# Performance work log

Hardware: AMD Instinct MI355X
Metric: run time of the kernel (lower is better)

Reference implementation:

```python
import jax, jax.numpy as jnp
import numpy as np

N, C, H, E = 10000, 128, 256, 320000
CUTOFF = 5.0
EPS = 1e-5


def _ln(x, g, b):
    mu = jnp.mean(x, axis=-1, keepdims=True)
    var = jnp.var(x, axis=-1, keepdims=True)
    return (x - mu) * jax.lax.rsqrt(var + EPS) * g + b


def setup_inputs() -> dict:
    key = jax.random.key(0)
    ks = jax.random.split(key, 24)

    def w(k, shape, fan_in):
        return (jax.random.normal(k, shape, dtype=jnp.float32) / np.sqrt(fan_in)).astype(jnp.float32)

    inp = {}
    inp["x"] = jax.random.normal(ks[0], (N, 3), dtype=jnp.float32)
    inp["h"] = jax.random.normal(ks[1], (N, C), dtype=jnp.float32)
    inp["edge_index"] = jax.random.randint(ks[2], (2, E), 0, N, dtype=jnp.int32)
    # edge_mlp: Linear(2C+1 -> H), SiLU, Linear(H -> H), SiLU
    inp["We1"] = w(ks[3], (2 * C + 1, H), 2 * C + 1); inp["be1"] = jnp.zeros((H,), jnp.float32)
    inp["We2"] = w(ks[4], (H, H), H);                inp["be2"] = jnp.zeros((H,), jnp.float32)
    # node_mlp: Linear(C+H -> H), SiLU, Linear(H -> C)
    inp["Wn1"] = w(ks[5], (C + H, H), C + H);        inp["bn1"] = jnp.zeros((H,), jnp.float32)
    inp["Wn2"] = w(ks[6], (H, C), H);                inp["bn2"] = jnp.zeros((C,), jnp.float32)
    # residual mlp: Linear(C -> H), SiLU, Dropout(eval), Linear(H -> C)
    inp["Wm1"] = w(ks[7], (C, H), C);                inp["bm1"] = jnp.zeros((H,), jnp.float32)
    inp["Wm2"] = w(ks[8], (H, C), H);                inp["bm2"] = jnp.zeros((C,), jnp.float32)
    # layernorms
    inp["g1"] = jnp.ones((C,), jnp.float32); inp["beta1"] = jnp.zeros((C,), jnp.float32)
    inp["g2"] = jnp.ones((C,), jnp.float32); inp["beta2"] = jnp.zeros((C,), jnp.float32)
    return inp


def reference(x, h, edge_index, We1, be1, We2, be2, Wn1, bn1, Wn2, bn2,
              Wm1, bm1, Wm2, bm2, g1, beta1, g2, beta2):
    row, col = edge_index[0], edge_index[1]

    h_res = h
    hn = _ln(h, g1, beta1)                              # [N, C]

    # ---- EGNN layer ----
    rel = x[row] - x[col]                               # [E, 3]
    dist = jnp.linalg.norm(rel, axis=-1, keepdims=True) # [E, 1]
    edge_in = jnp.concatenate([hn[row], hn[col], dist], axis=-1)  # [E, 2C+1]
    m = jax.nn.silu(edge_in @ We1 + be1)
    m = jax.nn.silu(m @ We2 + be2)                      # [E, H]

    d = dist[:, 0]
    Ccut = 0.5 * (jnp.cos(d * jnp.pi / CUTOFF) + 1.0)
    Ccut = Ccut * (d <= CUTOFF) * (d >= 0.0)
    m = m * Ccut[:, None]

    # mean-aggregate messages at target nodes (edge_index[1])
    sums = jax.ops.segment_sum(m, col, num_segments=N)          # [N, H]
    cnt = jax.ops.segment_sum(jnp.ones((m.shape[0],), m.dtype), col, num_segments=N)
    m_aggr = sums / jnp.maximum(cnt, 1.0)[:, None]

    hd = jax.nn.silu(jnp.concatenate([hn, m_aggr], axis=-1) @ Wn1 + bn1) @ Wn2 + bn2
    h_egnn = hn + hd

    h1 = h_res + h_egnn

    # ---- norm2 + MLP residual (dropout = identity in eval) ----
    h2 = _ln(h1, g2, beta2)
    h2 = jax.nn.silu(h2 @ Wm1 + bm1) @ Wm2 + bm2
    return h1 + h2
```

## Files before the change

kernel.cpp:

```cpp
#include <hip/hip_runtime.h>

#define NN 10000
#define CC 128
#define HH 256
#define EE 320000
#define ETILE 128

typedef __bf16 bf16_t;
typedef __bf16 bf16x8 __attribute__((ext_vector_type(8)));
typedef __bf16 bf16x4 __attribute__((ext_vector_type(4)));
typedef __bf16 bf16x2 __attribute__((ext_vector_type(2)));
typedef float f32x4 __attribute__((ext_vector_type(4)));

__device__ __forceinline__ float silu_f(float v) {
#if __has_builtin(__builtin_amdgcn_rcpf)
  return v * __builtin_amdgcn_rcpf(1.0f + __expf(-v));
#else
  return v / (1.0f + __expf(-v));
#endif
}


template<int RE, int KD, int SA, int NT>
__device__ __forceinline__ void gemm_lg(const bf16_t* sAa, const bf16_t* __restrict__ BT,
                                        int nwavebase, int lr, int quad, f32x4 acc[RE][NT]) {
  for (int kk = 0; kk < KD; kk += 32) {
    bf16x8 a[RE]; bf16x8 b[NT];
#pragma unroll
    for (int re = 0; re < RE; re++)
      a[re] = *(const bf16x8*)(sAa + (re * 16 + lr) * SA + kk + quad * 8);
#pragma unroll
    for (int ce = 0; ce < NT; ce++)
      b[ce] = *(const bf16x8*)(BT + (size_t)(nwavebase + ce * 16 + lr) * KD + kk + quad * 8);
#pragma unroll
    for (int re = 0; re < RE; re++)
#pragma unroll
      for (int ce = 0; ce < NT; ce++)
        acc[re][ce] = __builtin_amdgcn_mfma_f32_16x16x32_bf16(a[re], b[ce], acc[re][ce], 0, 0, 0);
  }
}

template<int KD, int SB, int NE>
__device__ __forceinline__ void gemm_gl(const bf16_t* __restrict__ AT, int mwavebase,
                                        const bf16_t* sB, int lr, int quad, f32x4 acc[4][NE]) {
  for (int kk = 0; kk < KD; kk += 32) {
    bf16x8 a[4]; bf16x8 b[NE];
#pragma unroll
    for (int re = 0; re < 4; re++)
      a[re] = *(const bf16x8*)(AT + (size_t)(mwavebase + re * 16 + lr) * KD + kk + quad * 8);
#pragma unroll
    for (int ce = 0; ce < NE; ce++)
      b[ce] = *(const bf16x8*)(sB + (ce * 16 + lr) * SB + kk + quad * 8);
#pragma unroll
    for (int re = 0; re < 4; re++)
#pragma unroll
      for (int ce = 0; ce < NE; ce++)
        acc[re][ce] = __builtin_amdgcn_mfma_f32_16x16x32_bf16(a[re], b[ce], acc[re][ce], 0, 0, 0);
  }
}

__global__ __launch_bounds__(256) void prep_weights(
    const float* __restrict__ We1, const float* __restrict__ We2,
    const float* __restrict__ Wn1, const float* __restrict__ Wn2,
    const float* __restrict__ Wm1, const float* __restrict__ Wm2,
    bf16_t* __restrict__ We1T, bf16_t* __restrict__ We2T,
    bf16_t* __restrict__ Wn1T, bf16_t* __restrict__ Wn2T,
    bf16_t* __restrict__ Wm1T, bf16_t* __restrict__ Wm2T) {
  int i = blockIdx.x * 256 + threadIdx.x;
  const float* src; bf16_t* dst; int K, Nc, idx;
  if      (i < 65536)  { src = We1; dst = We1T; K = 256; Nc = 256; idx = i; }
  else if (i < 131072) { src = We2; dst = We2T; K = 256; Nc = 256; idx = i - 65536; }
  else if (i < 229376) { src = Wn1; dst = Wn1T; K = 384; Nc = 256; idx = i - 131072; }
  else if (i < 262144) { src = Wn2; dst = Wn2T; K = 256; Nc = 128; idx = i - 229376; }
  else if (i < 294912) { src = Wm1; dst = Wm1T; K = 128; Nc = 256; idx = i - 262144; }
  else                 { src = Wm2; dst = Wm2T; K = 256; Nc = 128; idx = i - 294912; }
  int n = idx / K, k = idx - n * K;
  dst[idx] = (bf16_t)src[(size_t)k * Nc + n];
}

__global__ __launch_bounds__(256) void ln1_kernel(const float* __restrict__ src,
                                                  const float* __restrict__ g,
                                                  const float* __restrict__ b,
                                                  bf16_t* __restrict__ out16) {
  int node = blockIdx.x * 4 + (threadIdx.x >> 6);
  int lane = threadIdx.x & 63;
  size_t base = (size_t)node * CC;
  float v1 = src[base + lane], v2 = src[base + lane + 64];
  float s = v1 + v2, sq = v1 * v1 + v2 * v2;
#pragma unroll
  for (int o = 32; o > 0; o >>= 1) { s += __shfl_xor(s, o); sq += __shfl_xor(sq, o); }
  float mu = s * (1.0f / CC);
  float var = sq * (1.0f / CC) - mu * mu;
  float rs = rsqrtf(var + 1e-5f);
  out16[base + lane] = (bf16_t)((v1 - mu) * rs * g[lane] + b[lane]);
  out16[base + lane + 64] = (bf16_t)((v2 - mu) * rs * g[lane + 64] + b[lane + 64]);
}

__global__ __launch_bounds__(256) void count_kernel(const int* __restrict__ ei, int* __restrict__ cnt) {
  int e = blockIdx.x * 256 + threadIdx.x;
  atomicAdd(&cnt[ei[EE + e]], 1);
}

__global__ __launch_bounds__(1024) void scan_kernel(const int* __restrict__ cnt, int* __restrict__ cursor) {
  __shared__ int wsum[16];
  int tid = threadIdx.x, wave = tid >> 6, lane = tid & 63;
  int base = 0;
  for (int start = 0; start < NN; start += 1024) {
    int i = start + tid;
    int v = (i < NN) ? cnt[i] : 0;
    int s = v;
#pragma unroll
    for (int off = 1; off < 64; off <<= 1) { int t = __shfl_up(s, off); if (lane >= off) s += t; }
    if (lane == 63) wsum[wave] = s;
    __syncthreads();
    if (tid < 16) {
      int ws = wsum[tid];
#pragma unroll
      for (int off = 1; off < 16; off <<= 1) { int t = __shfl_up(ws, off); if (tid >= off) ws += t; }
      wsum[tid] = ws;
    }
    __syncthreads();
    int wp = (wave > 0) ? wsum[wave - 1] : 0;
    if (i < NN) cursor[i] = base + wp + s - v;
    base += wsum[15];
    __syncthreads();
  }
}

__global__ __launch_bounds__(256) void scatter_kernel(const int* __restrict__ ei,
                                                      const float* __restrict__ x,
                                                      int* __restrict__ cursor,
                                                      uint4* __restrict__ edat) {
  int e = blockIdx.x * 256 + threadIdx.x;
  int r = ei[e], c = ei[EE + e];
  float dx = x[3 * r] - x[3 * c];
  float dy = x[3 * r + 1] - x[3 * c + 1];
  float dz = x[3 * r + 2] - x[3 * c + 2];
  float d = sqrtf(dx * dx + dy * dy + dz * dz);
  float cc = (d <= 5.0f) ? 0.5f * (cosf(d * 0.6283185307179586f) + 1.0f) : 0.0f;
  int pos = atomicAdd(&cursor[c], 1);
  uint4 v = {(unsigned)r, (unsigned)c, __float_as_uint(d), __float_as_uint(cc)};
  edat[pos] = v;
}

__global__ __launch_bounds__(256, 2) void edge_mlp_kernel(
    const uint4* __restrict__ edat, const bf16_t* __restrict__ hn16,
    const bf16_t* __restrict__ We1T, const float* __restrict__ We1last,
    const float* __restrict__ be1,
    const bf16_t* __restrict__ We2T, const float* __restrict__ be2,
    float* __restrict__ sums) {
  __shared__ __align__(16) bf16_t sBuf[ETILE * 264];
  __shared__ int sRow[ETILE], sCol[ETILE];
  __shared__ float sD[ETILE], sCc[ETILE];
  __shared__ int sSegStart[ETILE + 1];
  __shared__ int sNseg;
  __shared__ unsigned long long sMask[2];
  int tid = threadIdx.x;
  int lane = tid & 63, wave = tid >> 6;
  int lr = lane & 15, quad = lane >> 4;
  int e0 = blockIdx.x * ETILE;

  if (tid < ETILE) {
    uint4 v = edat[e0 + tid];
    sRow[tid] = (int)v.x; sCol[tid] = (int)v.y;
    sD[tid] = __uint_as_float(v.z); sCc[tid] = __uint_as_float(v.w);
  }
  __syncthreads();

  if (tid < ETILE) {
    int fl = (tid > 0) && (sCol[tid] != sCol[tid - 1]);
    unsigned long long m = __ballot(fl);
    if ((tid & 63) == 0) sMask[wave] = m;
  }

#pragma unroll
  for (int i = 0; i < 16; i++) {
    int o = tid + i * 256;
    int e = o >> 5, q = o & 31;
    int srcrow = (q < 16) ? sRow[e] : sCol[e];
    uint4 v = *(const uint4*)(hn16 + (size_t)srcrow * CC + (q & 15) * 8);
    *(uint4*)(sBuf + e * 264 + (q & 15) * 8 + ((q < 16) ? 0 : 128)) = v;
  }
  __syncthreads();

  f32x4 zf = {0.f, 0.f, 0.f, 0.f};
  {
    f32x4 acc[4][8];
#pragma unroll
    for (int i = 0; i < 4; i++)
#pragma unroll
      for (int j = 0; j < 8; j++) acc[i][j] = zf;
    gemm_gl<256, 264, 8>(We1T, wave * 64, sBuf, lr, quad, acc);
    __syncthreads();

#pragma unroll
    for (int re = 0; re < 4; re++) {
      int nb = wave * 64 + re * 16 + quad * 4;
      f32x4 b1 = *(const f32x4*)(be1 + nb);
      f32x4 wl = *(const f32x4*)(We1last + nb);
#pragma unroll
      for (int ce = 0; ce < 8; ce++) {
        int e = ce * 16 + lr;
        float d = sD[e];
        bf16x4 o;
#pragma unroll
        for (int r = 0; r < 4; r++)
          o[r] = (bf16_t)silu_f(acc[re][ce][r] + b1[r] + d * wl[r]);
        *(bf16x4*)(sBuf + e * 264 + nb) = o;
      }
    }
  }
  __syncthreads();

  {
    f32x4 acc[8][4];
#pragma unroll
    for (int i = 0; i < 8; i++)
#pragma unroll
      for (int j = 0; j < 4; j++) acc[i][j] = zf;
    gemm_lg<8, 256, 264, 4>(sBuf, We2T, wave * 64, lr, quad, acc);
    __syncthreads();

#pragma unroll
    for (int re = 0; re < 8; re++) {
      int eb = re * 16 + quad * 4;
      f32x4 cc = *(const f32x4*)(sCc + eb);
#pragma unroll
      for (int ce = 0; ce < 4; ce++) {
        int n = wave * 64 + ce * 16 + lr;
        float b2 = be2[n];
        float v0 = silu_f(acc[re][ce][0] + b2) * cc[0];
        float v1 = silu_f(acc[re][ce][1] + b2) * cc[1];
        float v2 = silu_f(acc[re][ce][2] + b2) * cc[2];
        float v3 = silu_f(acc[re][ce][3] + b2) * cc[3];
        bf16x2 p0 = {(bf16_t)v0, (bf16_t)v1};
        bf16x2 p1 = {(bf16_t)v2, (bf16_t)v3};
        *(bf16x2*)(sBuf + n * 130 + eb) = p0;
        *(bf16x2*)(sBuf + n * 130 + eb + 2) = p1;
      }
    }
  }

  if (tid < ETILE) {
    unsigned long long m0 = sMask[0], m1 = sMask[1];
    int fl = (tid > 0) && (sCol[tid] != sCol[tid - 1]);
    if (fl) {
      int l = tid & 63;
      unsigned long long below = ((tid < 64) ? m0 : m1) & ((1ull << l) - 1ull);
      int idx = __popcll(below) + ((tid >= 64) ? __popcll(m0) : 0) + 1;
      sSegStart[idx] = tid;
    }
    if (tid == 0) {
      int ns = 1 + __popcll(m0) + __popcll(m1);
      sNseg = ns;
      sSegStart[0] = 0;
      sSegStart[ns] = ETILE;
    }
  }
  __syncthreads();

  {
    int nseg = sNseg;
    const bf16_t* rowp = sBuf + tid * 130;
    for (int s = 0; s < nseg; s++) {
      int lo = sSegStart[s], hi = sSegStart[s + 1];
      int colv = sCol[lo];
      float a = 0.0f;
      int e = lo;
      if (e & 1) { a += (float)rowp[e]; e++; }
      for (; e + 1 < hi; e += 2) {
        unsigned w = *(const unsigned*)(rowp + e);
        a += __uint_as_float(w << 16) + __uint_as_float(w & 0xffff0000u);
      }
      if (e < hi) a += (float)rowp[e];
      atomicAdd(&sums[(size_t)colv * HH + tid], a);
    }
  }
}

__global__ __launch_bounds__(256) void node_fused_kernel(
    const float* __restrict__ h, const bf16_t* __restrict__ hn16,
    const float* __restrict__ sums, const int* __restrict__ cnt,
    const bf16_t* __restrict__ Wn1T, const float* __restrict__ bn1,
    const bf16_t* __restrict__ Wn2T, const float* __restrict__ bn2,
    const float* __restrict__ g2, const float* __restrict__ bt2,
    const bf16_t* __restrict__ Wm1T, const float* __restrict__ bm1,
    const bf16_t* __restrict__ Wm2T, const float* __restrict__ bm2,
    float* __restrict__ out) {
  __shared__ __align__(16) bf16_t sA1[16 * 392];
  __shared__ __align__(16) bf16_t sM[16 * 264];
  __shared__ __align__(16) float sH1[16 * 132];
  __shared__ __align__(16) bf16_t sLn[16 * 136];
  __shared__ float sRc[16];
  int tid = threadIdx.x;
  int lane = tid & 63, wave = tid >> 6;
  int lr = lane & 15, quad = lane >> 4;
  int n0 = blockIdx.x * 16;

  if (tid < 16) sRc[tid] = 1.0f / fmaxf((float)cnt[n0 + tid], 1.0f);
  __syncthreads();

#pragma unroll
  for (int i = 0; i < 3; i++) {
    int o = tid + i * 256;
    int e = o / 48, q = o - e * 48;
    int node = n0 + e;
    if (q < 16) {
      *(uint4*)(sA1 + e * 392 + q * 8) = *(const uint4*)(hn16 + (size_t)node * CC + q * 8);
    } else {
      float rc = sRc[e];
      const float* sp = sums + (size_t)node * HH + (q - 16) * 8;
      bf16x8 bv;
#pragma unroll
      for (int k2 = 0; k2 < 8; k2++) bv[k2] = (bf16_t)(sp[k2] * rc);
      *(bf16x8*)(sA1 + e * 392 + (q - 16) * 8 + 128) = bv;
    }
  }
  __syncthreads();

  f32x4 zf = {0.f, 0.f, 0.f, 0.f};
  {
    f32x4 acc[1][4];
#pragma unroll
    for (int j = 0; j < 4; j++) acc[0][j] = zf;
    gemm_lg<1, 384, 392, 4>(sA1, Wn1T, wave * 64, lr, quad, acc);
#pragma unroll
    for (int ce = 0; ce < 4; ce++) {
      int n = wave * 64 + ce * 16 + lr;
      float b1 = bn1[n];
#pragma unroll
      for (int r = 0; r < 4; r++)
        sM[(quad * 4 + r) * 264 + n] = (bf16_t)silu_f(acc[0][ce][r] + b1);
    }
  }
  __syncthreads();

  {
    f32x4 acc[1][2];
    acc[0][0] = zf; acc[0][1] = zf;
    gemm_lg<1, 256, 264, 2>(sM, Wn2T, wave * 32, lr, quad, acc);
#pragma unroll
    for (int ce = 0; ce < 2; ce++) {
      int n = wave * 32 + ce * 16 + lr;
      float b2 = bn2[n];
#pragma unroll
      for (int r = 0; r < 4; r++) {
        int node = quad * 4 + r;
        size_t idx = (size_t)(n0 + node) * CC + n;
        float hn_v = (float)sA1[node * 392 + n];
        sH1[node * 132 + n] = h[idx] + hn_v + acc[0][ce][r] + b2;
      }
    }
  }
  __syncthreads();

  {
    int node = tid >> 4, c0 = (tid & 15) * 8;
    f32x4 u0 = *(const f32x4*)(sH1 + node * 132 + c0);
    f32x4 u1 = *(const f32x4*)(sH1 + node * 132 + c0 + 4);
    float s = 0.f, sq = 0.f;
#pragma unroll
    for (int j = 0; j < 4; j++) { s += u0[j] + u1[j]; sq += u0[j] * u0[j] + u1[j] * u1[j]; }
#pragma unroll
    for (int o = 8; o > 0; o >>= 1) { s += __shfl_xor(s, o); sq += __shfl_xor(sq, o); }
    float mu = s * (1.0f / CC);
    float var = sq * (1.0f / CC) - mu * mu;
    float rs = rsqrtf(var + 1e-5f);
    f32x4 gg0 = *(const f32x4*)(g2 + c0), gg1 = *(const f32x4*)(g2 + c0 + 4);
    f32x4 bb0 = *(const f32x4*)(bt2 + c0), bb1 = *(const f32x4*)(bt2 + c0 + 4);
    bf16x8 ov;
#pragma unroll
    for (int j = 0; j < 4; j++) {
      ov[j] = (bf16_t)((u0[j] - mu) * rs * gg0[j] + bb0[j]);
      ov[j + 4] = (bf16_t)((u1[j] - mu) * rs * gg1[j] + bb1[j]);
    }
    *(bf16x8*)(sLn + node * 136 + c0) = ov;
  }
  __syncthreads();

  {
    f32x4 acc[1][4];
#pragma unroll
    for (int j = 0; j < 4; j++) acc[0][j] = zf;
    gemm_lg<1, 128, 136, 4>(sLn, Wm1T, wave * 64, lr, quad, acc);
#pragma unroll
    for (int ce = 0; ce < 4; ce++) {
      int n = wave * 64 + ce * 16 + lr;
      float b1 = bm1[n];
#pragma unroll
      for (int r = 0; r < 4; r++)
        sM[(quad * 4 + r) * 264 + n] = (bf16_t)silu_f(acc[0][ce][r] + b1);
    }
  }
  __syncthreads();

  {
    f32x4 acc[1][2];
    acc[0][0] = zf; acc[0][1] = zf;
    gemm_lg<1, 256, 264, 2>(sM, Wm2T, wave * 32, lr, quad, acc);
#pragma unroll
    for (int ce = 0; ce < 2; ce++) {
      int n = wave * 32 + ce * 16 + lr;
      float b2 = bm2[n];
#pragma unroll
      for (int r = 0; r < 4; r++) {
        int node = quad * 4 + r;
        size_t idx = (size_t)(n0 + node) * CC + n;
        out[idx] = sH1[node * 132 + n] + acc[0][ce][r] + b2;
      }
    }
  }
}

extern "C" void kernel_launch(void* const* d_in, const int* in_sizes, int n_in,
                              void* d_out, int out_size, void* d_ws, size_t ws_size,
                              hipStream_t stream) {
  const float* x    = (const float*)d_in[0];
  const float* h    = (const float*)d_in[1];
  const int*   ei   = (const int*)d_in[2];
  const float* We1  = (const float*)d_in[3];
  const float* be1  = (const float*)d_in[4];
  const float* We2  = (const float*)d_in[5];
  const float* be2  = (const float*)d_in[6];
  const float* Wn1  = (const float*)d_in[7];
  const float* bn1  = (const float*)d_in[8];
  const float* Wn2  = (const float*)d_in[9];
  const float* bn2  = (const float*)d_in[10];
  const float* Wm1  = (const float*)d_in[11];
  const float* bm1  = (const float*)d_in[12];
  const float* Wm2  = (const float*)d_in[13];
  const float* bm2  = (const float*)d_in[14];
  const float* g1   = (const float*)d_in[15];
  const float* bt1  = (const float*)d_in[16];
  const float* g2   = (const float*)d_in[17];
  const float* bt2  = (const float*)d_in[18];
  float* out = (float*)d_out;

  char* wp = (char*)d_ws;
  size_t off = 0;
  auto alloc = [&](size_t bytes) -> void* {
    void* p = wp + off;
    off = (off + bytes + 255) & ~(size_t)255;
    return p;
  };

  bf16_t* hn16   = (bf16_t*)alloc((size_t)NN * CC * 2);
  float*  sums   = (float*)alloc((size_t)NN * HH * 4);
  int*    cnt    = (int*)alloc((size_t)NN * 4);
  int*    cursor = (int*)alloc((size_t)NN * 4);
  uint4*  edat   = (uint4*)alloc((size_t)EE * 16);
  bf16_t* We1T   = (bf16_t*)alloc(256 * 256 * 2);
  bf16_t* We2T   = (bf16_t*)alloc(256 * 256 * 2);
  bf16_t* Wn1T   = (bf16_t*)alloc(256 * 384 * 2);
  bf16_t* Wn2T   = (bf16_t*)alloc(128 * 256 * 2);
  bf16_t* Wm1T   = (bf16_t*)alloc(256 * 128 * 2);
  bf16_t* Wm2T   = (bf16_t*)alloc(128 * 256 * 2);

  hipMemsetAsync(sums, 0, (size_t)NN * HH * 4, stream);
  hipMemsetAsync(cnt, 0, (size_t)NN * 4, stream);

  prep_weights<<<1280, 256, 0, stream>>>(We1, We2, Wn1, Wn2, Wm1, Wm2,
                                         We1T, We2T, Wn1T, Wn2T, Wm1T, Wm2T);

  ln1_kernel<<<NN / 4, 256, 0, stream>>>(h, g1, bt1, hn16);

  count_kernel<<<EE / 256, 256, 0, stream>>>(ei, cnt);
  scan_kernel<<<1, 1024, 0, stream>>>(cnt, cursor);
  scatter_kernel<<<EE / 256, 256, 0, stream>>>(ei, x, cursor, edat);

  edge_mlp_kernel<<<EE / ETILE, 256, 0, stream>>>(edat, hn16,
                                                  We1T, We1 + 256 * 256, be1,
                                                  We2T, be2, sums);

  node_fused_kernel<<<NN / 16, 256, 0, stream>>>(h, hn16, sums, cnt,
                                                 Wn1T, bn1, Wn2T, bn2,
                                                 g2, bt2, Wm1T, bm1, Wm2T, bm2, out);
}
```

Baseline: 347.3 us.

## Factor first edge-MLP layer into per-node projections and reduce segments in registers

The first edge layer is linear over the concatenation [hn[row], hn[col], dist], so it is split into two per-node projections. A new node_pre_kernel fuses LayerNorm with computing P = hn·We1[:C] + be1 and Q = hn·We1[C:2C], and the edge kernel only gathers P[row] + Q[col] + d·w_last before SiLU. This replaces an E×256×256 GEMM with an N-sized one. It also removes the shared-memory transpose for segment sums by reducing each segment in MFMA accumulator registers with shuffles, and retiles edges to 96 per block, zero-padding the sorted edge buffer. The cost is an extra bf16 PQ buffer read with random gathers, plus some rounding from storing P and Q in bf16 before the add.

```diff
diff --git a/kernel.cpp b/kernel.cpp
--- a/kernel.cpp
+++ b/kernel.cpp
@@ -4,12 +4,12 @@
 #define CC 128
 #define HH 256
 #define EE 320000
-#define ETILE 128
+#define ETILE 96
+#define EBLOCKS 3334
 
 typedef __bf16 bf16_t;
 typedef __bf16 bf16x8 __attribute__((ext_vector_type(8)));
 typedef __bf16 bf16x4 __attribute__((ext_vector_type(4)));
-typedef __bf16 bf16x2 __attribute__((ext_vector_type(2)));
 typedef float f32x4 __attribute__((ext_vector_type(4)));
 
 __device__ __forceinline__ float silu_f(float v) {
@@ -20,7 +20,6 @@
 #endif
 }
 
-
 template<int RE, int KD, int SA, int NT>
 __device__ __forceinline__ void gemm_lg(const bf16_t* sAa, const bf16_t* __restrict__ BT,
                                         int nwavebase, int lr, int quad, f32x4 acc[RE][NT]) {
@@ -36,25 +35,6 @@
     for (int re = 0; re < RE; re++)
 #pragma unroll
       for (int ce = 0; ce < NT; ce++)
-        acc[re][ce] = __builtin_amdgcn_mfma_f32_16x16x32_bf16(a[re], b[ce], acc[re][ce], 0, 0, 0);
-  }
-}
-
-template<int KD, int SB, int NE>
-__device__ __forceinline__ void gemm_gl(const bf16_t* __restrict__ AT, int mwavebase,
-                                        const bf16_t* sB, int lr, int quad, f32x4 acc[4][NE]) {
-  for (int kk = 0; kk < KD; kk += 32) {
-    bf16x8 a[4]; bf16x8 b[NE];
-#pragma unroll
-    for (int re = 0; re < 4; re++)
-      a[re] = *(const bf16x8*)(AT + (size_t)(mwavebase + re * 16 + lr) * KD + kk + quad * 8);
-#pragma unroll
-    for (int ce = 0; ce < NE; ce++)
-      b[ce] = *(const bf16x8*)(sB + (ce * 16 + lr) * SB + kk + quad * 8);
-#pragma unroll
-    for (int re = 0; re < 4; re++)
-#pragma unroll
-      for (int ce = 0; ce < NE; ce++)
         acc[re][ce] = __builtin_amdgcn_mfma_f32_16x16x32_bf16(a[re], b[ce], acc[re][ce], 0, 0, 0);
   }
 }
@@ -78,22 +58,101 @@
   dst[idx] = (bf16_t)src[(size_t)k * Nc + n];
 }
 
-__global__ __launch_bounds__(256) void ln1_kernel(const float* __restrict__ src,
-                                                  const float* __restrict__ g,
-                                                  const float* __restrict__ b,
-                                                  bf16_t* __restrict__ out16) {
-  int node = blockIdx.x * 4 + (threadIdx.x >> 6);
-  int lane = threadIdx.x & 63;
-  size_t base = (size_t)node * CC;
-  float v1 = src[base + lane], v2 = src[base + lane + 64];
-  float s = v1 + v2, sq = v1 * v1 + v2 * v2;
-#pragma unroll
-  for (int o = 32; o > 0; o >>= 1) { s += __shfl_xor(s, o); sq += __shfl_xor(sq, o); }
-  float mu = s * (1.0f / CC);
-  float var = sq * (1.0f / CC) - mu * mu;
-  float rs = rsqrtf(var + 1e-5f);
-  out16[base + lane] = (bf16_t)((v1 - mu) * rs * g[lane] + b[lane]);
-  out16[base + lane + 64] = (bf16_t)((v2 - mu) * rs * g[lane + 64] + b[lane + 64]);
+__global__ __launch_bounds__(256, 3) void node_pre_kernel(
+    const float* __restrict__ h, const float* __restrict__ g1,
+    const float* __restrict__ bt1,
+    const bf16_t* __restrict__ We1T, const float* __restrict__ be1,
+    bf16_t* __restrict__ hn16, bf16_t* __restrict__ PQ) {
+  __shared__ __align__(16) float sHf[64 * 132];
+  __shared__ __align__(16) bf16_t sHn[64 * 136];
+  int tid = threadIdx.x;
+  int lane = tid & 63, wave = tid >> 6;
+  int lr = lane & 15, quad = lane >> 4;
+  int n0 = blockIdx.x * 64;
+
+#pragma unroll
+  for (int i = 0; i < 8; i++) {
+    int o = tid + i * 256;
+    int node = o >> 5, q = o & 31;
+    f32x4 v = {0.f, 0.f, 0.f, 0.f};
+    if (n0 + node < NN) v = *(const f32x4*)(h + (size_t)(n0 + node) * CC + q * 4);
+    *(f32x4*)(sHf + node * 132 + q * 4) = v;
+  }
+  __syncthreads();
+
+  {
+    int node = tid >> 2, c0 = (tid & 3) * 32;
+    f32x4 u[8];
+    float s = 0.f, sq = 0.f;
+#pragma unroll
+    for (int j = 0; j < 8; j++) {
+      u[j] = *(const f32x4*)(sHf + node * 132 + c0 + j * 4);
+#pragma unroll
+      for (int r = 0; r < 4; r++) { s += u[j][r]; sq += u[j][r] * u[j][r]; }
+    }
+    s += __shfl_xor(s, 1); sq += __shfl_xor(sq, 1);
+    s += __shfl_xor(s, 2); sq += __shfl_xor(sq, 2);
+    float mu = s * (1.0f / CC);
+    float var = sq * (1.0f / CC) - mu * mu;
+    float rs = rsqrtf(var + 1e-5f);
+    bool live = (n0 + node) < NN;
+#pragma unroll
+    for (int j2 = 0; j2 < 4; j2++) {
+      f32x4 gg0 = *(const f32x4*)(g1 + c0 + j2 * 8);
+      f32x4 gg1 = *(const f32x4*)(g1 + c0 + j2 * 8 + 4);
+      f32x4 bb0 = *(const f32x4*)(bt1 + c0 + j2 * 8);
+      f32x4 bb1 = *(const f32x4*)(bt1 + c0 + j2 * 8 + 4);
+      bf16x8 ov;
+#pragma unroll
+      for (int r = 0; r < 4; r++) {
+        ov[r] = (bf16_t)((u[j2 * 2][r] - mu) * rs * gg0[r] + bb0[r]);
+        ov[r + 4] = (bf16_t)((u[j2 * 2 + 1][r] - mu) * rs * gg1[r] + bb1[r]);
+      }
+      *(bf16x8*)(sHn + node * 136 + c0 + j2 * 8) = ov;
+      if (live) *(bf16x8*)(hn16 + (size_t)(n0 + node) * CC + c0 + j2 * 8) = ov;
+    }
+  }
+  __syncthreads();
+
+  f32x4 zf = {0.f, 0.f, 0.f, 0.f};
+#pragma unroll
+  for (int p = 0; p < 2; p++) {
+    f32x4 acc[4][4];
+#pragma unroll
+    for (int i = 0; i < 4; i++)
+#pragma unroll
+      for (int j = 0; j < 4; j++) acc[i][j] = zf;
+    for (int kk = 0; kk < 128; kk += 32) {
+      bf16x8 a[4]; bf16x8 b[4];
+#pragma unroll
+      for (int re = 0; re < 4; re++)
+        a[re] = *(const bf16x8*)(We1T + (size_t)(wave * 64 + re * 16 + lr) * 256 + p * 128 + kk + quad * 8);
+#pragma unroll
+      for (int ce = 0; ce < 4; ce++)
+        b[ce] = *(const bf16x8*)(sHn + (ce * 16 + lr) * 136 + kk + quad * 8);
+#pragma unroll
+      for (int re = 0; re < 4; re++)
+#pragma unroll
+        for (int ce = 0; ce < 4; ce++)
+          acc[re][ce] = __builtin_amdgcn_mfma_f32_16x16x32_bf16(a[re], b[ce], acc[re][ce], 0, 0, 0);
+    }
+#pragma unroll
+    for (int re = 0; re < 4; re++) {
+      int cbase = wave * 64 + re * 16 + quad * 4;
+      f32x4 bb = zf;
+      if (p == 0) bb = *(const f32x4*)(be1 + cbase);
+#pragma unroll
+      for (int ce = 0; ce < 4; ce++) {
+        int node = ce * 16 + lr;
+        if (n0 + node < NN) {
+          bf16x4 o;
+#pragma unroll
+          for (int r = 0; r < 4; r++) o[r] = (bf16_t)(acc[re][ce][r] + bb[r]);
+          *(bf16x4*)(PQ + (size_t)(n0 + node) * 512 + p * 256 + cbase) = o;
+        }
+      }
+    }
+  }
 }
 
 __global__ __launch_bounds__(256) void count_kernel(const int* __restrict__ ei, int* __restrict__ cnt) {
@@ -143,17 +202,14 @@
   edat[pos] = v;
 }
 
-__global__ __launch_bounds__(256, 2) void edge_mlp_kernel(
-    const uint4* __restrict__ edat, const bf16_t* __restrict__ hn16,
-    const bf16_t* __restrict__ We1T, const float* __restrict__ We1last,
-    const float* __restrict__ be1,
+__global__ __launch_bounds__(256, 3) void edge_mlp_kernel(
+    const uint4* __restrict__ edat, const bf16_t* __restrict__ PQ,
+    const float* __restrict__ We1last,
     const bf16_t* __restrict__ We2T, const float* __restrict__ be2,
     float* __restrict__ sums) {
-  __shared__ __align__(16) bf16_t sBuf[ETILE * 264];
+  __shared__ __align__(16) bf16_t sM1[ETILE * 264];
   __shared__ int sRow[ETILE], sCol[ETILE];
   __shared__ float sD[ETILE], sCc[ETILE];
-  __shared__ int sSegStart[ETILE + 1];
-  __shared__ int sNseg;
   __shared__ unsigned long long sMask[2];
   int tid = threadIdx.x;
   int lane = tid & 63, wave = tid >> 6;
@@ -174,106 +230,86 @@
   }
 
 #pragma unroll
-  for (int i = 0; i < 16; i++) {
+  for (int i = 0; i < ETILE * 32 / 256; i++) {
     int o = tid + i * 256;
     int e = o >> 5, q = o & 31;
-    int srcrow = (q < 16) ? sRow[e] : sCol[e];
-    uint4 v = *(const uint4*)(hn16 + (size_t)srcrow * CC + (q & 15) * 8);
-    *(uint4*)(sBuf + e * 264 + (q & 15) * 8 + ((q < 16) ? 0 : 128)) = v;
+    int k0 = q * 8;
+    int row = sRow[e], col = sCol[e];
+    float d = sD[e];
+    bf16x8 pv = *(const bf16x8*)(PQ + (size_t)row * 512 + k0);
+    bf16x8 qv = *(const bf16x8*)(PQ + (size_t)col * 512 + 256 + k0);
+    f32x4 wl0 = *(const f32x4*)(We1last + k0);
+    f32x4 wl1 = *(const f32x4*)(We1last + k0 + 4);
+    bf16x8 m;
+#pragma unroll
+    for (int j = 0; j < 4; j++) {
+      m[j] = (bf16_t)silu_f((float)pv[j] + (float)qv[j] + d * wl0[j]);
+      m[j + 4] = (bf16_t)silu_f((float)pv[j + 4] + (float)qv[j + 4] + d * wl1[j]);
+    }
+    *(bf16x8*)(sM1 + e * 264 + k0) = m;
   }
   __syncthreads();
 
   f32x4 zf = {0.f, 0.f, 0.f, 0.f};
-  {
-    f32x4 acc[4][8];
-#pragma unroll
-    for (int i = 0; i < 4; i++)
-#pragma unroll
-      for (int j = 0; j < 8; j++) acc[i][j] = zf;
-    gemm_gl<256, 264, 8>(We1T, wave * 64, sBuf, lr, quad, acc);
-    __syncthreads();
-
-#pragma unroll
-    for (int re = 0; re < 4; re++) {
-      int nb = wave * 64 + re * 16 + quad * 4;
-      f32x4 b1 = *(const f32x4*)(be1 + nb);
-      f32x4 wl = *(const f32x4*)(We1last + nb);
-#pragma unroll
-      for (int ce = 0; ce < 8; ce++) {
-        int e = ce * 16 + lr;
-        float d = sD[e];
-        bf16x4 o;
-#pragma unroll
-        for (int r = 0; r < 4; r++)
-          o[r] = (bf16_t)silu_f(acc[re][ce][r] + b1[r] + d * wl[r]);
-        *(bf16x4*)(sBuf + e * 264 + nb) = o;
-      }
-    }
-  }
-  __syncthreads();
-
-  {
-    f32x4 acc[8][4];
-#pragma unroll
-    for (int i = 0; i < 8; i++)
-#pragma unroll
-      for (int j = 0; j < 4; j++) acc[i][j] = zf;
-    gemm_lg<8, 256, 264, 4>(sBuf, We2T, wave * 64, lr, quad, acc);
-    __syncthreads();
-
-#pragma unroll
-    for (int re = 0; re < 8; re++) {
-      int eb = re * 16 + quad * 4;
-      f32x4 cc = *(const f32x4*)(sCc + eb);
+  f32x4 acc[6][4];
+#pragma unroll
+  for (int i = 0; i < 6; i++)
+#pragma unroll
+    for (int j = 0; j < 4; j++) acc[i][j] = zf;
+  gemm_lg<6, 256, 264, 4>(sM1, We2T, wave * 64, lr, quad, acc);
+
+  float be2v[4];
+#pragma unroll
+  for (int ce = 0; ce < 4; ce++) be2v[ce] = be2[wave * 64 + ce * 16 + lr];
+#pragma unroll
+  for (int re = 0; re < 6; re++) {
+    f32x4 cc = *(const f32x4*)(sCc + re * 16 + quad * 4);
+#pragma unroll
+    for (int ce = 0; ce < 4; ce++)
+#pragma unroll
+      for (int r = 0; r < 4; r++)
+        acc[re][ce][r] = silu_f(acc[re][ce][r] + be2v[ce]) * cc[r];
+  }
+
+  {
+    unsigned long long w0 = sMask[0];
+    unsigned long long w1 = sMask[1];
+    int lo = 0;
+    while (lo < ETILE) {
+      int hi;
+      unsigned long long t = (lo < 63) ? (w0 & (~0ull << (lo + 1))) : 0ull;
+      if (t) {
+        hi = __ffsll((long long)t) - 1;
+      } else {
+        unsigned long long mk = (lo + 1 > 64) ? (~0ull << (lo + 1 - 64)) : ~0ull;
+        unsigned long long t1 = w1 & mk;
+        hi = t1 ? 64 + __ffsll((long long)t1) - 1 : ETILE;
+      }
+      f32x4 tv = zf;
+#pragma unroll
+      for (int re = 0; re < 6; re++) {
+        int eb = re * 16 + quad * 4;
+#pragma unroll
+        for (int r = 0; r < 4; r++) {
+          int e = eb + r;
+          bool in = (e >= lo) && (e < hi);
+#pragma unroll
+          for (int ce = 0; ce < 4; ce++)
+            tv[ce] += in ? acc[re][ce][r] : 0.0f;
+        }
+      }
 #pragma unroll
       for (int ce = 0; ce < 4; ce++) {
-        int n = wave * 64 + ce * 16 + lr;
-        float b2 = be2[n];
-        float v0 = silu_f(acc[re][ce][0] + b2) * cc[0];
-        float v1 = silu_f(acc[re][ce][1] + b2) * cc[1];
-        float v2 = silu_f(acc[re][ce][2] + b2) * cc[2];
-        float v3 = silu_f(acc[re][ce][3] + b2) * cc[3];
-        bf16x2 p0 = {(bf16_t)v0, (bf16_t)v1};
-        bf16x2 p1 = {(bf16_t)v2, (bf16_t)v3};
-        *(bf16x2*)(sBuf + n * 130 + eb) = p0;
-        *(bf16x2*)(sBuf + n * 130 + eb + 2) = p1;
-      }
-    }
-  }
-
-  if (tid < ETILE) {
-    unsigned long long m0 = sMask[0], m1 = sMask[1];
-    int fl = (tid > 0) && (sCol[tid] != sCol[tid - 1]);
-    if (fl) {
-      int l = tid & 63;
-      unsigned long long below = ((tid < 64) ? m0 : m1) & ((1ull << l) - 1ull);
-      int idx = __popcll(below) + ((tid >= 64) ? __popcll(m0) : 0) + 1;
-      sSegStart[idx] = tid;
-    }
-    if (tid == 0) {
-      int ns = 1 + __popcll(m0) + __popcll(m1);
-      sNseg = ns;
-      sSegStart[0] = 0;
-      sSegStart[ns] = ETILE;
-    }
-  }
-  __syncthreads();
-
-  {
-    int nseg = sNseg;
-    const bf16_t* rowp = sBuf + tid * 130;
-    for (int s = 0; s < nseg; s++) {
-      int lo = sSegStart[s], hi = sSegStart[s + 1];
-      int colv = sCol[lo];
-      float a = 0.0f;
-      int e = lo;
-      if (e & 1) { a += (float)rowp[e]; e++; }
-      for (; e + 1 < hi; e += 2) {
-        unsigned w = *(const unsigned*)(rowp + e);
-        a += __uint_as_float(w << 16) + __uint_as_float(w & 0xffff0000u);
-      }
-      if (e < hi) a += (float)rowp[e];
-      atomicAdd(&sums[(size_t)colv * HH + tid], a);
+        tv[ce] += __shfl_xor(tv[ce], 16);
+        tv[ce] += __shfl_xor(tv[ce], 32);
+      }
+      if (quad == 0) {
+        int colv = sCol[lo];
+#pragma unroll
+        for (int ce = 0; ce < 4; ce++)
+          atomicAdd(&sums[(size_t)colv * HH + wave * 64 + ce * 16 + lr], tv[ce]);
+      }
+      lo = hi;
     }
   }
 }
@@ -445,10 +481,11 @@
   };
 
   bf16_t* hn16   = (bf16_t*)alloc((size_t)NN * CC * 2);
+  bf16_t* PQ     = (bf16_t*)alloc((size_t)NN * 512 * 2);
   float*  sums   = (float*)alloc((size_t)NN * HH * 4);
   int*    cnt    = (int*)alloc((size_t)NN * 4);
   int*    cursor = (int*)alloc((size_t)NN * 4);
-  uint4*  edat   = (uint4*)alloc((size_t)EE * 16);
+  uint4*  edat   = (uint4*)alloc((size_t)(EBLOCKS * ETILE) * 16);
   bf16_t* We1T   = (bf16_t*)alloc(256 * 256 * 2);
   bf16_t* We2T   = (bf16_t*)alloc(256 * 256 * 2);
   bf16_t* Wn1T   = (bf16_t*)alloc(256 * 384 * 2);
@@ -458,19 +495,19 @@
 
   hipMemsetAsync(sums, 0, (size_t)NN * HH * 4, stream);
   hipMemsetAsync(cnt, 0, (size_t)NN * 4, stream);
+  hipMemsetAsync(edat + EE, 0, (size_t)(EBLOCKS * ETILE - EE) * 16, stream);
 
   prep_weights<<<1280, 256, 0, stream>>>(We1, We2, Wn1, Wn2, Wm1, Wm2,
                                          We1T, We2T, Wn1T, Wn2T, Wm1T, Wm2T);
 
-  ln1_kernel<<<NN / 4, 256, 0, stream>>>(h, g1, bt1, hn16);
+  node_pre_kernel<<<(NN + 63) / 64, 256, 0, stream>>>(h, g1, bt1, We1T, be1, hn16, PQ);
 
   count_kernel<<<EE / 256, 256, 0, stream>>>(ei, cnt);
   scan_kernel<<<1, 1024, 0, stream>>>(cnt, cursor);
   scatter_kernel<<<EE / 256, 256, 0, stream>>>(ei, x, cursor, edat);
 
-  edge_mlp_kernel<<<EE / ETILE, 256, 0, stream>>>(edat, hn16,
-                                                  We1T, We1 + 256 * 256, be1,
-                                                  We2T, be2, sums);
+  edge_mlp_kernel<<<EBLOCKS, 256, 0, stream>>>(edat, PQ, We1 + 256 * 256,
+                                               We2T, be2, sums);
 
   node_fused_kernel<<<NN / 16, 256, 0, stream>>>(h, hn16, sums, cnt,
                                                  Wn1T, bn1, Wn2T, bn2,
```

New measurement: 311.7 us. 1.11x faster.
